# Kernel optimization log

Hardware: AMD Instinct MI355X
Metric: run time of the kernel (lower is better)

## Reference

```python
import jax, jax.numpy as jnp
import numpy as np

N_NODES = 100000
N_EDGES = 1000000
DIM = 64
N_GRAPHS = 256
OUT_DIM = 10
BN_EPS = 1e-5


def setup_inputs() -> dict:
    key = jax.random.key(0)
    ks = jax.random.split(key, 12)
    s = 0.1  # weight init scale
    x = jax.random.normal(ks[0], (N_NODES, DIM), jnp.float32)
    edge_index = jax.random.randint(ks[1], (2, N_EDGES), 0, N_NODES, dtype=jnp.int32)
    batch = jnp.sort(jax.random.randint(ks[2], (N_NODES,), 0, N_GRAPHS, dtype=jnp.int32))
    w1 = jax.random.normal(ks[3], (3, DIM, DIM), jnp.float32) * s
    b1 = jax.random.normal(ks[4], (3, DIM), jnp.float32) * s
    w2 = jax.random.normal(ks[5], (3, DIM, DIM), jnp.float32) * s
    b2 = jax.random.normal(ks[6], (3, DIM), jnp.float32) * s
    gamma = jax.random.uniform(ks[7], (3, DIM), jnp.float32, 0.5, 1.5)
    beta = jax.random.normal(ks[8], (3, DIM), jnp.float32) * s
    eps_g = jnp.zeros((3,), jnp.float32)  # GIN train_eps, init 0
    lin_w = jax.random.normal(ks[9], (DIM, OUT_DIM), jnp.float32) * s
    lin_b = jax.random.normal(ks[10], (OUT_DIM,), jnp.float32) * s
    return dict(x=x, edge_index=edge_index, batch=batch, w1=w1, b1=b1,
                w2=w2, b2=b2, gamma=gamma, beta=beta, eps_g=eps_g,
                lin_w=lin_w, lin_b=lin_b)


def _gin_layer(x, src, dst, w1, b1, w2, b2, gamma, beta, eps):
    # scatter-add neighbor aggregation: agg[i] = sum_{(j->i) in E} x[j]
    agg = jax.ops.segment_sum(x[src], dst, num_segments=N_NODES)
    h = (1.0 + eps) * x + agg
    h = jax.nn.relu(h @ w1 + b1)
    h = jax.nn.relu(h @ w2 + b2)
    # BatchNorm1d, training-mode batch statistics (biased variance)
    mean = jnp.mean(h, axis=0)
    var = jnp.mean((h - mean) ** 2, axis=0)
    h = (h - mean) * jax.lax.rsqrt(var + BN_EPS) * gamma + beta
    return jax.nn.relu(h)  # outer F.relu(conv(...))


def reference(x, edge_index, batch, w1, b1, w2, b2, gamma, beta, eps_g, lin_w, lin_b):
    src, dst = edge_index[0], edge_index[1]
    for i in range(3):
        x = _gin_layer(x, src, dst, w1[i], b1[i], w2[i], b2[i],
                       gamma[i], beta[i], eps_g[i])
    # global mean pool over graphs
    sums = jax.ops.segment_sum(x, batch, num_segments=N_GRAPHS)
    counts = jax.ops.segment_sum(jnp.ones((x.shape[0],), x.dtype), batch,
                                 num_segments=N_GRAPHS)
    pooled = sums / jnp.maximum(counts, 1.0)[:, None]
    return pooled @ lin_w + lin_b
```

## Files before the change

kernel.cpp:

```cpp
#include <hip/hip_runtime.h>
#include <hip/hip_bf16.h>

#define N_NODES 100000
#define N_EDGES 1000000
#define DIM 64
#define N_GRAPHS 256
#define OUT_DIM 10
#define BN_EPS 1e-5f

#define POOL_BLOCKS 512
#define LAYER_BLOCKS ((N_NODES + 63) / 64)
#define PAD 24
#define SPILL_CAP 8192
#define NPART 8
#define PART_SZ ((N_NODES + NPART - 1) / NPART)

typedef __bf16 bf16x8 __attribute__((ext_vector_type(8)));
typedef float f32x4 __attribute__((ext_vector_type(4)));

__global__ __launch_bounds__(256) void fill_kernel(
    const int* __restrict__ ei, int* __restrict__ deg,
    int* __restrict__ esrc, int* __restrict__ nspill, int* __restrict__ spill)
{
    const int part = blockIdx.x & (NPART - 1);
    const int e = (blockIdx.x >> 3) * 256 + threadIdx.x;
    if (e >= N_EDGES) return;
    int dst = ei[N_EDGES + e];
    int lo = part * PART_SZ;
    if (dst < lo || dst >= lo + PART_SZ) return;
    int src = ei[e];
    int pos = atomicAdd(&deg[dst], 1);
    if (pos < PAD) {
        esrc[dst * PAD + pos] = src;
    } else {
        int sp = atomicAdd(nspill, 1);
        if (sp < SPILL_CAP) { spill[2 * sp] = dst; spill[2 * sp + 1] = src; }
    }
}

__global__ __launch_bounds__(256) void xcast_kernel(
    const float4* __restrict__ xin, ushort4* __restrict__ xout)
{
    int t = blockIdx.x * 256 + threadIdx.x;
    if (t >= N_NODES * 16) return;
    float4 v = xin[t];
    ushort4 o;
    o.x = __builtin_bit_cast(unsigned short, (__bf16)v.x);
    o.y = __builtin_bit_cast(unsigned short, (__bf16)v.y);
    o.z = __builtin_bit_cast(unsigned short, (__bf16)v.z);
    o.w = __builtin_bit_cast(unsigned short, (__bf16)v.w);
    xout[t] = o;
}

__global__ __launch_bounds__(64) void bnprep_kernel(
    const float* __restrict__ sums, const float* __restrict__ gamma,
    const float* __restrict__ beta, float* __restrict__ sc)
{
    int d = threadIdx.x;
    const float inv_n = 1.0f / (float)N_NODES;
    float mean = sums[d] * inv_n;
    float m2 = sums[64 + d] * inv_n;
    float var = m2 - mean * mean;
    float scale = gamma[d] * rsqrtf(var + BN_EPS);
    sc[d] = scale;
    sc[64 + d] = fmaf(-mean, scale, beta[d]);
}

__global__ __launch_bounds__(256) void wprep_kernel(
    const float* __restrict__ w1, const float* __restrict__ w2,
    __bf16* __restrict__ wf)
{
    int L = blockIdx.x >> 1, mat = blockIdx.x & 1;
    const float* w = (mat ? w2 : w1) + L * 4096;
    __bf16* dst = wf + blockIdx.x * 8192;
#pragma unroll
    for (int r = 0; r < 2; ++r) {
        int idx = threadIdx.x + 256 * r;
        int lane = idx & 63;
        int kt = idx >> 6;
        int kstep = kt >> 2, nt = kt & 3;
        int n = nt * 16 + (lane & 15);
        int kbase = kstep * 32 + (lane >> 4) * 8;
#pragma unroll
        for (int j = 0; j < 8; ++j) {
            float v = w[(kbase + j) * 64 + n];
            __bf16 hi = (__bf16)v;
            dst[idx * 8 + j] = hi;
            dst[4096 + idx * 8 + j] = (__bf16)(v - (float)hi);
        }
    }
}

template <bool BN>
__global__ __launch_bounds__(256) void layer_kernel(
    const float* __restrict__ x, const unsigned short* __restrict__ xb,
    const float* __restrict__ sc,
    const int* __restrict__ deg, const int* __restrict__ esrc,
    const int* __restrict__ nspill, const int* __restrict__ spill,
    float* __restrict__ h2out, unsigned short* __restrict__ xbout,
    const __bf16* __restrict__ wf1, const __bf16* __restrict__ wf2,
    const float* __restrict__ b1, const float* __restrict__ b2,
    const float* __restrict__ eps_all, int layer,
    float* __restrict__ sums)
{
    __shared__ __attribute__((aligned(16))) unsigned tile[4][16][68];
    __shared__ float bnacc[128];

    const int tid = threadIdx.x;
    const int lane = tid & 63;
    const int wv = tid >> 6;
    const int q = lane >> 4;
    const int r = lane & 15;
    const int node0 = blockIdx.x * 64 + wv * 16;
    const bool active = node0 < N_NODES;

    if (tid < 128) bnacc[tid] = 0.0f;

    f32x4 acc[4];
    float bs[4], bq[4];
#pragma unroll
    for (int nt = 0; nt < 4; ++nt) {
        acc[nt] = (f32x4){0.f, 0.f, 0.f, 0.f};
        bs[nt] = 0.0f; bq[nt] = 0.0f;
    }

    float scale = 1.0f, shift = 0.0f;
    if (BN) { scale = sc[lane]; shift = sc[64 + lane]; }

    if (active) {
        const float epsv = 1.0f + eps_all[layer];

        int dvec = 0;
        if (lane < 16) dvec = deg[node0 + lane];
        uint4 nf0, nf1, nf2;
        {
            const uint4* ip = (const uint4*)(esrc + (size_t)node0 * PAD);
            nf0 = ip[0]; nf1 = ip[1]; nf2 = ip[2];
        }
        for (int i = 0; i < 16; ++i) {
            const uint4 c0 = nf0, c1 = nf1, c2 = nf2;
            if (i < 15) {
                const uint4* ip = (const uint4*)(esrc + (size_t)(node0 + i + 1) * PAD);
                nf0 = ip[0]; nf1 = ip[1]; nf2 = ip[2];
            }
            const int n = node0 + i;
            const int dfull = __builtin_amdgcn_readlane(dvec, i);
            const int d = min(dfull, PAD);

            float xv = x[(size_t)n * 64 + lane];
            if (BN) xv = fmaxf(fmaf(xv, scale, shift), 0.0f);
            float hval = epsv * xv;

            {
                unsigned idx[12] = {c0.x, c0.y, c0.z, c0.w, c1.x, c1.y,
                                    c1.z, c1.w, c2.x, c2.y, c2.z, c2.w};
                unsigned short u[12];
#pragma unroll
                for (int j = 0; j < 12; ++j) {
                    unsigned s = idx[j];
                    s = (s < (unsigned)N_NODES) ? s : 0u;
                    u[j] = xb[(size_t)s * 64 + lane];
                }
#pragma unroll
                for (int j = 0; j < 12; ++j) {
                    float t = (float)__builtin_bit_cast(__bf16, u[j]);
                    if (BN) t = fmaxf(fmaf(t, scale, shift), 0.0f);
                    hval += (j < d) ? t : 0.0f;
                }
            }
            if (d > 12) {
                const int* ep = esrc + (size_t)n * PAD + 12;
                unsigned short u[12];
#pragma unroll
                for (int j = 0; j < 12; ++j) {
                    unsigned s = (unsigned)ep[j];
                    s = (s < (unsigned)N_NODES) ? s : 0u;
                    u[j] = xb[(size_t)s * 64 + lane];
                }
#pragma unroll
                for (int j = 0; j < 12; ++j) {
                    float t = (float)__builtin_bit_cast(__bf16, u[j]);
                    if (BN) t = fmaxf(fmaf(t, scale, shift), 0.0f);
                    hval += (12 + j < d) ? t : 0.0f;
                }
            }
            if (dfull > PAD) {
                int ns = min(*nspill, SPILL_CAP);
                for (int e = 0; e < ns; ++e) {
                    if (spill[2 * e] == n) {
                        float t = (float)__builtin_bit_cast(
                            __bf16, xb[(size_t)spill[2 * e + 1] * 64 + lane]);
                        if (BN) t = fmaxf(fmaf(t, scale, shift), 0.0f);
                        hval += t;
                    }
                }
            }
            __bf16 hi = (__bf16)hval;
            __bf16 lo = (__bf16)(hval - (float)hi);
            tile[wv][i][lane] = ((unsigned)__builtin_bit_cast(unsigned short, hi) << 16)
                              | (unsigned)__builtin_bit_cast(unsigned short, lo);
        }

        uint4 f0 = *(const uint4*)&tile[wv][r][q * 8];
        uint4 f1 = *(const uint4*)&tile[wv][r][q * 8 + 4];
        uint4 f2 = *(const uint4*)&tile[wv][r][32 + q * 8];
        uint4 f3 = *(const uint4*)&tile[wv][r][32 + q * 8 + 4];
#pragma unroll
        for (int kstep = 0; kstep < 2; ++kstep) {
            uint4 p0 = kstep ? f2 : f0;
            uint4 p1 = kstep ? f3 : f1;
            unsigned pk[8] = {p0.x, p0.y, p0.z, p0.w, p1.x, p1.y, p1.z, p1.w};
            bf16x8 ahi, alo;
#pragma unroll
            for (int j = 0; j < 8; ++j) {
                ahi[j] = __builtin_bit_cast(__bf16, (unsigned short)(pk[j] >> 16));
                alo[j] = __builtin_bit_cast(__bf16, (unsigned short)(pk[j] & 0xffffu));
            }
#pragma unroll
            for (int nt = 0; nt < 4; ++nt) {
                const __bf16* bp = wf1 + ((kstep * 4 + nt) * 64 + lane) * 8;
                bf16x8 bhi = *(const bf16x8*)bp;
                bf16x8 blo = *(const bf16x8*)(bp + 4096);
                acc[nt] = __builtin_amdgcn_mfma_f32_16x16x32_bf16(ahi, bhi, acc[nt], 0, 0, 0);
                acc[nt] = __builtin_amdgcn_mfma_f32_16x16x32_bf16(alo, bhi, acc[nt], 0, 0, 0);
                acc[nt] = __builtin_amdgcn_mfma_f32_16x16x32_bf16(ahi, blo, acc[nt], 0, 0, 0);
            }
        }
#pragma unroll
        for (int nt = 0; nt < 4; ++nt) {
            float b1v = b1[nt * 16 + r];
#pragma unroll
            for (int reg = 0; reg < 4; ++reg) {
                float v = fmaxf(acc[nt][reg] + b1v, 0.0f);
                __bf16 hi = (__bf16)v;
                __bf16 lo = (__bf16)(v - (float)hi);
                unsigned pk = ((unsigned)__builtin_bit_cast(unsigned short, hi) << 16)
                            | (unsigned)__builtin_bit_cast(unsigned short, lo);
                tile[wv][q * 4 + reg][nt * 16 + r] = pk;
            }
            acc[nt] = (f32x4){0.f, 0.f, 0.f, 0.f};
        }
#pragma unroll
        for (int kstep = 0; kstep < 2; ++kstep) {
            uint4 p0 = *(const uint4*)&tile[wv][r][kstep * 32 + q * 8];
            uint4 p1 = *(const uint4*)&tile[wv][r][kstep * 32 + q * 8 + 4];
            unsigned pk[8] = {p0.x, p0.y, p0.z, p0.w, p1.x, p1.y, p1.z, p1.w};
            bf16x8 ahi, alo;
#pragma unroll
            for (int j = 0; j < 8; ++j) {
                ahi[j] = __builtin_bit_cast(__bf16, (unsigned short)(pk[j] >> 16));
                alo[j] = __builtin_bit_cast(__bf16, (unsigned short)(pk[j] & 0xffffu));
            }
#pragma unroll
            for (int nt = 0; nt < 4; ++nt) {
                const __bf16* bp = wf2 + ((kstep * 4 + nt) * 64 + lane) * 8;
                bf16x8 bhi = *(const bf16x8*)bp;
                bf16x8 blo = *(const bf16x8*)(bp + 4096);
                acc[nt] = __builtin_amdgcn_mfma_f32_16x16x32_bf16(ahi, bhi, acc[nt], 0, 0, 0);
                acc[nt] = __builtin_amdgcn_mfma_f32_16x16x32_bf16(alo, bhi, acc[nt], 0, 0, 0);
                acc[nt] = __builtin_amdgcn_mfma_f32_16x16x32_bf16(ahi, blo, acc[nt], 0, 0, 0);
            }
        }
#pragma unroll
        for (int nt = 0; nt < 4; ++nt) {
            float b2v = b2[nt * 16 + r];
#pragma unroll
            for (int reg = 0; reg < 4; ++reg) {
                float v = fmaxf(acc[nt][reg] + b2v, 0.0f);
                size_t oi = (size_t)(node0 + q * 4 + reg) * 64 + nt * 16 + r;
                h2out[oi] = v;
                xbout[oi] = __builtin_bit_cast(unsigned short, (__bf16)v);
                bs[nt] += v;
                bq[nt] = fmaf(v, v, bq[nt]);
            }
        }
    }
    __syncthreads();
#pragma unroll
    for (int nt = 0; nt < 4; ++nt) {
        float s = bs[nt];
        s += __shfl_xor(s, 16);
        s += __shfl_xor(s, 32);
        float ss = bq[nt];
        ss += __shfl_xor(ss, 16);
        ss += __shfl_xor(ss, 32);
        if (q == 0) {
            atomicAdd(&bnacc[nt * 16 + r], s);
            atomicAdd(&bnacc[64 + nt * 16 + r], ss);
        }
    }
    __syncthreads();
    if (tid < 128) unsafeAtomicAdd(&sums[tid], bnacc[tid]);
}

__global__ __launch_bounds__(256) void pool_kernel(
    const float* __restrict__ h2, const float* __restrict__ sc,
    const int* __restrict__ batch,
    float* __restrict__ pooled, float* __restrict__ counts)
{
    const int lane = threadIdx.x & 63;
    const int w = blockIdx.x * 4 + (threadIdx.x >> 6);
    const int nw = POOL_BLOCKS * 4;
    const int npw = (N_NODES + nw - 1) / nw;
    int n0 = w * npw;
    if (n0 >= N_NODES) return;
    int n1 = n0 + npw;
    if (n1 > N_NODES) n1 = N_NODES;

    const float scale = sc[lane];
    const float shift = sc[64 + lane];

    int cur = batch[n0];
    float acc = 0.0f, cnt = 0.0f;
    for (int n = n0; n < n1; ++n) {
        int g = batch[n];
        if (g != cur) {
            unsafeAtomicAdd(&pooled[cur * 64 + lane], acc);
            if (lane == 0) unsafeAtomicAdd(&counts[cur], cnt);
            acc = 0.0f; cnt = 0.0f; cur = g;
        }
        float v = h2[(size_t)n * 64 + lane];
        v = fmaxf(fmaf(v, scale, shift), 0.0f);
        acc += v;
        cnt += 1.0f;
    }
    unsafeAtomicAdd(&pooled[cur * 64 + lane], acc);
    if (lane == 0) unsafeAtomicAdd(&counts[cur], cnt);
}

__global__ __launch_bounds__(256) void final_kernel(
    const float* __restrict__ pooled, const float* __restrict__ counts,
    const float* __restrict__ lin_w, const float* __restrict__ lin_b,
    float* __restrict__ out)
{
    int t = blockIdx.x * 256 + threadIdx.x;
    if (t >= N_GRAPHS * OUT_DIM) return;
    int g = t / OUT_DIM;
    int o = t - g * OUT_DIM;
    float acc = 0.0f;
#pragma unroll 8
    for (int d = 0; d < 64; ++d)
        acc = fmaf(pooled[g * 64 + d], lin_w[d * OUT_DIM + o], acc);
    float c = fmaxf(counts[g], 1.0f);
    out[t] = acc / c + lin_b[o];
}

extern "C" void kernel_launch(void* const* d_in, const int* in_sizes, int n_in,
                              void* d_out, int out_size, void* d_ws, size_t ws_size,
                              hipStream_t stream)
{
    const float* x0    = (const float*)d_in[0];
    const int*   ei    = (const int*)d_in[1];
    const int*   batch = (const int*)d_in[2];
    const float* w1    = (const float*)d_in[3];
    const float* b1    = (const float*)d_in[4];
    const float* w2    = (const float*)d_in[5];
    const float* b2    = (const float*)d_in[6];
    const float* gamma = (const float*)d_in[7];
    const float* beta  = (const float*)d_in[8];
    const float* eps_g = (const float*)d_in[9];
    const float* lin_w = (const float*)d_in[10];
    const float* lin_b = (const float*)d_in[11];
    float* out = (float*)d_out;

    float* ws   = (float*)d_ws;
    float* A    = ws;
    float* B    = ws + (size_t)N_NODES * 64;
    float* SUMS = ws + (size_t)2 * N_NODES * 64;
    float* POOL = SUMS + 384;
    float* CNT  = POOL + N_GRAPHS * 64;
    int*   DEG    = (int*)(CNT + N_GRAPHS);
    int*   NSPILL = DEG + N_NODES;
    float* SC   = (float*)(NSPILL + 16);
    __bf16* WF  = (__bf16*)(SC + 384);
    int*   SPILL  = (int*)(WF + 6 * 8192);
    int*   ESRC   = SPILL + 2 * SPILL_CAP;
    unsigned short* XP = (unsigned short*)(ESRC + (size_t)N_NODES * PAD);
    unsigned short* XQ = XP + (size_t)N_NODES * 64;
    unsigned short* XR = XQ + (size_t)N_NODES * 64;

    const size_t zero_bytes = (384 + N_GRAPHS * 64 + N_GRAPHS) * sizeof(float)
                            + (N_NODES + 16) * sizeof(int);
    const int fill_blocks = ((N_EDGES + 255) / 256) * NPART;
    const int elem_blocks = (N_NODES * 16 + 255) / 256;

    hipMemsetAsync(SUMS, 0, zero_bytes, stream);
    wprep_kernel<<<6, 256, 0, stream>>>(w1, w2, WF);
    xcast_kernel<<<elem_blocks, 256, 0, stream>>>((const float4*)x0, (ushort4*)XP);
    fill_kernel<<<fill_blocks, 256, 0, stream>>>(ei, DEG, ESRC, NSPILL, SPILL);

    layer_kernel<false><<<LAYER_BLOCKS, 256, 0, stream>>>(
        x0, XP, nullptr, DEG, ESRC, NSPILL, SPILL, A, XQ,
        WF, WF + 8192, b1, b2, eps_g, 0, SUMS);
    bnprep_kernel<<<1, 64, 0, stream>>>(SUMS, gamma, beta, SC);

    layer_kernel<true><<<LAYER_BLOCKS, 256, 0, stream>>>(
        A, XQ, SC, DEG, ESRC, NSPILL, SPILL, B, XP,
        WF + 16384, WF + 24576, b1 + 64, b2 + 64, eps_g, 1, SUMS + 128);
    bnprep_kernel<<<1, 64, 0, stream>>>(SUMS + 128, gamma + 64, beta + 64, SC + 128);

    layer_kernel<true><<<LAYER_BLOCKS, 256, 0, stream>>>(
        B, XP, SC + 128, DEG, ESRC, NSPILL, SPILL, A, XR,
        WF + 32768, WF + 40960, b1 + 128, b2 + 128, eps_g, 2, SUMS + 256);
    bnprep_kernel<<<1, 64, 0, stream>>>(SUMS + 256, gamma + 128, beta + 128, SC + 256);

    pool_kernel<<<POOL_BLOCKS, 256, 0, stream>>>(A, SC + 256, batch, POOL, CNT);
    final_kernel<<<(N_GRAPHS * OUT_DIM + 255) / 256, 256, 0, stream>>>(
        POOL, CNT, lin_w, lin_b, out);
}
```

Measured before the change: 398.2 us.

## Fold BN prep into consumers, gather bf16 pairs, skip final fp32 store

Removes the three single-block bnprep launches by having each layer kernel and the pool kernel compute the BatchNorm scale and shift from the running sums. The neighbor gather now has each half-wave load two bf16 features per lane for alternating neighbors, then combines the halves with a cross-lane shuffle. This halves the gather load instructions per node. The last layer no longer writes its fp32 output, and pooling reads the bf16 copy instead, which cuts write and read traffic but pools slightly less precise values.

```diff
diff --git a/kernel.cpp b/kernel.cpp
--- a/kernel.cpp
+++ b/kernel.cpp
@@ -17,6 +17,10 @@
 
 typedef __bf16 bf16x8 __attribute__((ext_vector_type(8)));
 typedef float f32x4 __attribute__((ext_vector_type(4)));
+
+__device__ __forceinline__ float bfu(unsigned short u) {
+    return (float)__builtin_bit_cast(__bf16, u);
+}
 
 __global__ __launch_bounds__(256) void fill_kernel(
     const int* __restrict__ ei, int* __restrict__ deg,
@@ -52,20 +56,6 @@
     xout[t] = o;
 }
 
-__global__ __launch_bounds__(64) void bnprep_kernel(
-    const float* __restrict__ sums, const float* __restrict__ gamma,
-    const float* __restrict__ beta, float* __restrict__ sc)
-{
-    int d = threadIdx.x;
-    const float inv_n = 1.0f / (float)N_NODES;
-    float mean = sums[d] * inv_n;
-    float m2 = sums[64 + d] * inv_n;
-    float var = m2 - mean * mean;
-    float scale = gamma[d] * rsqrtf(var + BN_EPS);
-    sc[d] = scale;
-    sc[64 + d] = fmaf(-mean, scale, beta[d]);
-}
-
 __global__ __launch_bounds__(256) void wprep_kernel(
     const float* __restrict__ w1, const float* __restrict__ w2,
     __bf16* __restrict__ wf)
@@ -91,17 +81,18 @@
     }
 }
 
-template <bool BN>
+template <bool BN, bool STORE32>
 __global__ __launch_bounds__(256) void layer_kernel(
     const float* __restrict__ x, const unsigned short* __restrict__ xb,
-    const float* __restrict__ sc,
+    const float* __restrict__ sums_in, const float* __restrict__ gamma,
+    const float* __restrict__ beta,
     const int* __restrict__ deg, const int* __restrict__ esrc,
     const int* __restrict__ nspill, const int* __restrict__ spill,
     float* __restrict__ h2out, unsigned short* __restrict__ xbout,
     const __bf16* __restrict__ wf1, const __bf16* __restrict__ wf2,
     const float* __restrict__ b1, const float* __restrict__ b2,
     const float* __restrict__ eps_all, int layer,
-    float* __restrict__ sums)
+    float* __restrict__ sums_out)
 {
     __shared__ __attribute__((aligned(16))) unsigned tile[4][16][68];
     __shared__ float bnacc[128];
@@ -109,6 +100,8 @@
     const int tid = threadIdx.x;
     const int lane = tid & 63;
     const int wv = tid >> 6;
+    const int half = lane >> 5;
+    const int c = lane & 31;
     const int q = lane >> 4;
     const int r = lane & 15;
     const int node0 = blockIdx.x * 64 + wv * 16;
@@ -116,6 +109,19 @@
 
     if (tid < 128) bnacc[tid] = 0.0f;
 
+    float sc0 = 1.0f, sc1 = 1.0f, sh0 = 0.0f, sh1 = 0.0f;
+    if (BN) {
+        const float inv_n = 1.0f / (float)N_NODES;
+        float m0 = sums_in[2 * c] * inv_n;
+        float m1 = sums_in[2 * c + 1] * inv_n;
+        float v0 = sums_in[64 + 2 * c] * inv_n - m0 * m0;
+        float v1 = sums_in[64 + 2 * c + 1] * inv_n - m1 * m1;
+        sc0 = gamma[2 * c] * rsqrtf(v0 + BN_EPS);
+        sc1 = gamma[2 * c + 1] * rsqrtf(v1 + BN_EPS);
+        sh0 = fmaf(-m0, sc0, beta[2 * c]);
+        sh1 = fmaf(-m1, sc1, beta[2 * c + 1]);
+    }
+
     f32x4 acc[4];
     float bs[4], bq[4];
 #pragma unroll
@@ -123,9 +129,6 @@
         acc[nt] = (f32x4){0.f, 0.f, 0.f, 0.f};
         bs[nt] = 0.0f; bq[nt] = 0.0f;
     }
-
-    float scale = 1.0f, shift = 0.0f;
-    if (BN) { scale = sc[lane]; shift = sc[64 + lane]; }
 
     if (active) {
         const float epsv = 1.0f + eps_all[layer];
@@ -147,58 +150,85 @@
             const int dfull = __builtin_amdgcn_readlane(dvec, i);
             const int d = min(dfull, PAD);
 
-            float xv = x[(size_t)n * 64 + lane];
-            if (BN) xv = fmaxf(fmaf(xv, scale, shift), 0.0f);
-            float hval = epsv * xv;
-
+            float hx = 0.0f, hy = 0.0f;
+            if (half == 0) {
+                float2 xv = *(const float2*)(x + (size_t)n * 64 + 2 * c);
+                if (BN) {
+                    xv.x = fmaxf(fmaf(xv.x, sc0, sh0), 0.0f);
+                    xv.y = fmaxf(fmaf(xv.y, sc1, sh1), 0.0f);
+                }
+                hx = epsv * xv.x;
+                hy = epsv * xv.y;
+            }
             {
                 unsigned idx[12] = {c0.x, c0.y, c0.z, c0.w, c1.x, c1.y,
                                     c1.z, c1.w, c2.x, c2.y, c2.z, c2.w};
-                unsigned short u[12];
-#pragma unroll
-                for (int j = 0; j < 12; ++j) {
-                    unsigned s = idx[j];
+                unsigned uv[6];
+#pragma unroll
+                for (int t = 0; t < 6; ++t) {
+                    unsigned s = idx[2 * t + half];
                     s = (s < (unsigned)N_NODES) ? s : 0u;
-                    u[j] = xb[(size_t)s * 64 + lane];
-                }
-#pragma unroll
-                for (int j = 0; j < 12; ++j) {
-                    float t = (float)__builtin_bit_cast(__bf16, u[j]);
-                    if (BN) t = fmaxf(fmaf(t, scale, shift), 0.0f);
-                    hval += (j < d) ? t : 0.0f;
+                    uv[t] = *(const unsigned*)(xb + (size_t)s * 64 + 2 * c);
+                }
+#pragma unroll
+                for (int t = 0; t < 6; ++t) {
+                    float t0 = bfu((unsigned short)(uv[t] & 0xffffu));
+                    float t1 = bfu((unsigned short)(uv[t] >> 16));
+                    if (BN) {
+                        t0 = fmaxf(fmaf(t0, sc0, sh0), 0.0f);
+                        t1 = fmaxf(fmaf(t1, sc1, sh1), 0.0f);
+                    }
+                    bool on = (2 * t + half) < d;
+                    hx += on ? t0 : 0.0f;
+                    hy += on ? t1 : 0.0f;
                 }
             }
             if (d > 12) {
                 const int* ep = esrc + (size_t)n * PAD + 12;
-                unsigned short u[12];
-#pragma unroll
-                for (int j = 0; j < 12; ++j) {
-                    unsigned s = (unsigned)ep[j];
+                unsigned uv[6];
+#pragma unroll
+                for (int t = 0; t < 6; ++t) {
+                    unsigned s = (unsigned)ep[2 * t + half];
                     s = (s < (unsigned)N_NODES) ? s : 0u;
-                    u[j] = xb[(size_t)s * 64 + lane];
-                }
-#pragma unroll
-                for (int j = 0; j < 12; ++j) {
-                    float t = (float)__builtin_bit_cast(__bf16, u[j]);
-                    if (BN) t = fmaxf(fmaf(t, scale, shift), 0.0f);
-                    hval += (12 + j < d) ? t : 0.0f;
-                }
-            }
+                    uv[t] = *(const unsigned*)(xb + (size_t)s * 64 + 2 * c);
+                }
+#pragma unroll
+                for (int t = 0; t < 6; ++t) {
+                    float t0 = bfu((unsigned short)(uv[t] & 0xffffu));
+                    float t1 = bfu((unsigned short)(uv[t] >> 16));
+                    if (BN) {
+                        t0 = fmaxf(fmaf(t0, sc0, sh0), 0.0f);
+                        t1 = fmaxf(fmaf(t1, sc1, sh1), 0.0f);
+                    }
+                    bool on = (12 + 2 * t + half) < d;
+                    hx += on ? t0 : 0.0f;
+                    hy += on ? t1 : 0.0f;
+                }
+            }
+            hx += __shfl_xor(hx, 32);
+            hy += __shfl_xor(hy, 32);
             if (dfull > PAD) {
                 int ns = min(*nspill, SPILL_CAP);
                 for (int e = 0; e < ns; ++e) {
                     if (spill[2 * e] == n) {
-                        float t = (float)__builtin_bit_cast(
-                            __bf16, xb[(size_t)spill[2 * e + 1] * 64 + lane]);
-                        if (BN) t = fmaxf(fmaf(t, scale, shift), 0.0f);
-                        hval += t;
+                        unsigned u = *(const unsigned*)(
+                            xb + (size_t)spill[2 * e + 1] * 64 + 2 * c);
+                        float t0 = bfu((unsigned short)(u & 0xffffu));
+                        float t1 = bfu((unsigned short)(u >> 16));
+                        if (BN) {
+                            t0 = fmaxf(fmaf(t0, sc0, sh0), 0.0f);
+                            t1 = fmaxf(fmaf(t1, sc1, sh1), 0.0f);
+                        }
+                        hx += t0; hy += t1;
                     }
                 }
             }
+            float hval = half ? hy : hx;
             __bf16 hi = (__bf16)hval;
             __bf16 lo = (__bf16)(hval - (float)hi);
-            tile[wv][i][lane] = ((unsigned)__builtin_bit_cast(unsigned short, hi) << 16)
-                              | (unsigned)__builtin_bit_cast(unsigned short, lo);
+            tile[wv][i][2 * c + half] =
+                ((unsigned)__builtin_bit_cast(unsigned short, hi) << 16)
+                | (unsigned)__builtin_bit_cast(unsigned short, lo);
         }
 
         uint4 f0 = *(const uint4*)&tile[wv][r][q * 8];
@@ -268,7 +298,7 @@
             for (int reg = 0; reg < 4; ++reg) {
                 float v = fmaxf(acc[nt][reg] + b2v, 0.0f);
                 size_t oi = (size_t)(node0 + q * 4 + reg) * 64 + nt * 16 + r;
-                h2out[oi] = v;
+                if (STORE32) h2out[oi] = v;
                 xbout[oi] = __builtin_bit_cast(unsigned short, (__bf16)v);
                 bs[nt] += v;
                 bq[nt] = fmaf(v, v, bq[nt]);
@@ -290,11 +320,12 @@
         }
     }
     __syncthreads();
-    if (tid < 128) unsafeAtomicAdd(&sums[tid], bnacc[tid]);
+    if (tid < 128) unsafeAtomicAdd(&sums_out[tid], bnacc[tid]);
 }
 
 __global__ __launch_bounds__(256) void pool_kernel(
-    const float* __restrict__ h2, const float* __restrict__ sc,
+    const unsigned short* __restrict__ h2b, const float* __restrict__ sums,
+    const float* __restrict__ gamma, const float* __restrict__ beta,
     const int* __restrict__ batch,
     float* __restrict__ pooled, float* __restrict__ counts)
 {
@@ -307,8 +338,11 @@
     int n1 = n0 + npw;
     if (n1 > N_NODES) n1 = N_NODES;
 
-    const float scale = sc[lane];
-    const float shift = sc[64 + lane];
+    const float inv_n = 1.0f / (float)N_NODES;
+    float mean = sums[lane] * inv_n;
+    float var = sums[64 + lane] * inv_n - mean * mean;
+    const float scale = gamma[lane] * rsqrtf(var + BN_EPS);
+    const float shift = fmaf(-mean, scale, beta[lane]);
 
     int cur = batch[n0];
     float acc = 0.0f, cnt = 0.0f;
@@ -319,7 +353,7 @@
             if (lane == 0) unsafeAtomicAdd(&counts[cur], cnt);
             acc = 0.0f; cnt = 0.0f; cur = g;
         }
-        float v = h2[(size_t)n * 64 + lane];
+        float v = bfu(h2b[(size_t)n * 64 + lane]);
         v = fmaxf(fmaf(v, scale, shift), 0.0f);
         acc += v;
         cnt += 1.0f;
@@ -371,8 +405,7 @@
     float* CNT  = POOL + N_GRAPHS * 64;
     int*   DEG    = (int*)(CNT + N_GRAPHS);
     int*   NSPILL = DEG + N_NODES;
-    float* SC   = (float*)(NSPILL + 16);
-    __bf16* WF  = (__bf16*)(SC + 384);
+    __bf16* WF  = (__bf16*)(NSPILL + 16);
     int*   SPILL  = (int*)(WF + 6 * 8192);
     int*   ESRC   = SPILL + 2 * SPILL_CAP;
     unsigned short* XP = (unsigned short*)(ESRC + (size_t)N_NODES * PAD);
@@ -389,22 +422,21 @@
     xcast_kernel<<<elem_blocks, 256, 0, stream>>>((const float4*)x0, (ushort4*)XP);
     fill_kernel<<<fill_blocks, 256, 0, stream>>>(ei, DEG, ESRC, NSPILL, SPILL);
 
-    layer_kernel<false><<<LAYER_BLOCKS, 256, 0, stream>>>(
-        x0, XP, nullptr, DEG, ESRC, NSPILL, SPILL, A, XQ,
+    layer_kernel<false, true><<<LAYER_BLOCKS, 256, 0, stream>>>(
+        x0, XP, nullptr, nullptr, nullptr, DEG, ESRC, NSPILL, SPILL, A, XQ,
         WF, WF + 8192, b1, b2, eps_g, 0, SUMS);
-    bnprep_kernel<<<1, 64, 0, stream>>>(SUMS, gamma, beta, SC);
-
-    layer_kernel<true><<<LAYER_BLOCKS, 256, 0, stream>>>(
-        A, XQ, SC, DEG, ESRC, NSPILL, SPILL, B, XP,
+
+    layer_kernel<true, true><<<LAYER_BLOCKS, 256, 0, stream>>>(
+        A, XQ, SUMS, gamma, beta, DEG, ESRC, NSPILL, SPILL, B, XP,
         WF + 16384, WF + 24576, b1 + 64, b2 + 64, eps_g, 1, SUMS + 128);
-    bnprep_kernel<<<1, 64, 0, stream>>>(SUMS + 128, gamma + 64, beta + 64, SC + 128);
-
-    layer_kernel<true><<<LAYER_BLOCKS, 256, 0, stream>>>(
-        B, XP, SC + 128, DEG, ESRC, NSPILL, SPILL, A, XR,
+
+    layer_kernel<true, false><<<LAYER_BLOCKS, 256, 0, stream>>>(
+        B, XP, SUMS + 128, gamma + 64, beta + 64, DEG, ESRC, NSPILL, SPILL,
+        nullptr, XR,
         WF + 32768, WF + 40960, b1 + 128, b2 + 128, eps_g, 2, SUMS + 256);
-    bnprep_kernel<<<1, 64, 0, stream>>>(SUMS + 256, gamma + 128, beta + 128, SC + 256);
-
-    pool_kernel<<<POOL_BLOCKS, 256, 0, stream>>>(A, SC + 256, batch, POOL, CNT);
+
+    pool_kernel<<<POOL_BLOCKS, 256, 0, stream>>>(
+        XR, SUMS + 256, gamma + 128, beta + 128, batch, POOL, CNT);
     final_kernel<<<(N_GRAPHS * OUT_DIM + 255) / 256, 256, 0, stream>>>(
         POOL, CNT, lin_w, lin_b, out);
 }
```

Measured after the change: 429.6 us. +7.9%, slower.
